# Kernel tuning notes

Measured on AMD Instinct MI355X. Metric: run time of the kernel, lower is better.

## Reference

```python
import jax, jax.numpy as jnp
import numpy as np

B, C, D, W, H = 8, 256, 24, 24, 24
COUT = 256
EMBED = 128
HEADS = 8
WORD = 64
POOL = 3  # forward hardcodes adaptive_avg_pool3d(x, 3)


def setup_inputs() -> dict:
    key = jax.random.key(0)
    ks = jax.random.split(key, 12)
    s = lambda n: 1.0 / np.sqrt(n)
    return {
        "x": jax.random.normal(ks[0], (B, C, D, W, H), dtype=jnp.float32),
        "qk_w": jax.random.normal(ks[1], (2 * EMBED, POOL ** 3), dtype=jnp.float32) * s(POOL ** 3),
        "qk_b": jax.random.normal(ks[2], (2 * EMBED,), dtype=jnp.float32) * 0.02,
        "wq_w": jax.random.normal(ks[3], (HEADS * WORD, EMBED), dtype=jnp.float32) * s(EMBED),
        "wq_b": jax.random.normal(ks[4], (HEADS * WORD,), dtype=jnp.float32) * 0.02,
        "wk_w": jax.random.normal(ks[5], (HEADS * WORD, EMBED), dtype=jnp.float32) * s(EMBED),
        "wk_b": jax.random.normal(ks[6], (HEADS * WORD,), dtype=jnp.float32) * 0.02,
        "fch_w": jax.random.normal(ks[7], (1, HEADS), dtype=jnp.float32) * s(HEADS),
        "fch_b": jax.random.normal(ks[8], (1,), dtype=jnp.float32) * 0.02,
        "conv_w": jax.random.normal(ks[9], (COUT, C), dtype=jnp.float32) * s(C),
        "conv_b": jax.random.normal(ks[10], (COUT,), dtype=jnp.float32) * 0.02,
    }


def reference(x, qk_w, qk_b, wq_w, wq_b, wk_w, wk_b, fch_w, fch_b, conv_w, conv_b):
    b, c, d, w, h = x.shape
    # adaptive_avg_pool3d to 3x3x3 (exact: dims divisible by 3) -> [b, c, 27]
    xmean = x.reshape(b, c, POOL, d // POOL, POOL, w // POOL, POOL, h // POOL)
    xmean = xmean.mean(axis=(3, 5, 7)).reshape(b, c, POOL ** 3)
    # qk projection -> split into q, k of [b, c, embed]
    qk = xmean @ qk_w.T + qk_b                      # [b, c, 2*embed]
    qk = qk.reshape(b, c, 2, EMBED)
    q, k = qk[:, :, 0], qk[:, :, 1]
    # head projections -> [b, heads, c, word]
    q = (q @ wq_w.T + wq_b).reshape(b, c, HEADS, WORD).transpose(0, 2, 1, 3)
    k = (k @ wk_w.T + wk_b).reshape(b, c, HEADS, WORD).transpose(0, 2, 1, 3)
    # channel attention: scores over channels [b, heads, c, c]
    scores = jnp.einsum("bhcw,bhkw->bhck", q / jnp.sqrt(jnp.float32(WORD)), k)
    attn = jax.nn.softmax(scores, axis=-1)          # dropout is identity in eval
    # v is the raw spatial map [b, c, d*w*h]; broadcast over heads
    v = x.reshape(b, c, d * w * h)
    y = jnp.einsum("bhck,bkn->bhcn", attn, v)       # [b, heads, c, dwh]
    # fch: Linear(heads, 1) combining heads
    y = jnp.einsum("bhcn,h->bcn", y, fch_w[0]) + fch_b[0]
    y = y.reshape(b, c, d, w, h)
    attn_out = jnp.einsum("bhck,h->bck", attn, fch_w[0]) + fch_b[0]  # [b, c, c]
    # 1x1x1 conv residual
    out = jnp.einsum("bcxyz,oc->boxyz", y + x, conv_w) + conv_b[None, :, None, None, None]
    return (out, attn_out)
```

## Files before the change

kernel.cpp:

```cpp
#include <hip/hip_runtime.h>
#include <cstdint>
#include <cstddef>

#define B_    8
#define C_    256
#define DWH   13824
#define P3    27
#define COUT_ 256

#define OFF_XMEAN 0
#define OFF_WQT   55296
#define OFF_WKT   69120
#define OFF_BQ    82944
#define OFF_BK    83456
#define OFF_BETA  83968
#define OFF_G     84224
#define OFF_U     90272
#define OFF_V     90488
#define OFF_D     90704
#define OFF_ZT    90712
#define OFF_A     549464
#define OFF_MPH   1073752
#define OFF_MPL   1335896

typedef __attribute__((ext_vector_type(8))) short bf16x8;
typedef __attribute__((ext_vector_type(4))) float f32x4;

__device__ __forceinline__ void split_bf16(float v, unsigned short& h, unsigned short& l) {
    unsigned u  = __float_as_uint(v);
    unsigned hu = u & 0xFFFF0000u;
    float r = v - __uint_as_float(hu);
    h = (unsigned short)(u >> 16);
    l = (unsigned short)(__float_as_uint(r) >> 16);
}

__device__ __forceinline__ unsigned rne2(float a, float b) {
    unsigned ua = __float_as_uint(a), ub = __float_as_uint(b);
    unsigned ra = (ua + 0x7FFFu + ((ua >> 16) & 1u)) >> 16;
    unsigned rb = (ub + 0x7FFFu + ((ub >> 16) & 1u)) >> 16;
    return ra | (rb << 16);
}

__global__ __launch_bounds__(256) void k_pool(const float* __restrict__ x,
                                              float* __restrict__ xmean) {
    int bc = blockIdx.x;
    __shared__ float p0[576], p1[576], p2[576];
    const float* xb = x + (size_t)bc * DWH;
    for (int t = threadIdx.x; t < 576; t += 256) {
        int g  = t >> 6;
        int s  = t & 63;
        int pd = g / 3, pw = g % 3;
        int d  = pd * 8 + (s >> 3);
        int w  = pw * 8 + (s & 7);
        const float4* r = (const float4*)(xb + ((size_t)d * 24 + w) * 24);
        float4 f0 = r[0], f1 = r[1], f2 = r[2], f3 = r[3], f4v = r[4], f5 = r[5];
        p0[t] = f0.x + f0.y + f0.z + f0.w + f1.x + f1.y + f1.z + f1.w;
        p1[t] = f2.x + f2.y + f2.z + f2.w + f3.x + f3.y + f3.z + f3.w;
        p2[t] = f4v.x + f4v.y + f4v.z + f4v.w + f5.x + f5.y + f5.z + f5.w;
    }
    __syncthreads();
    int tid = threadIdx.x;
    if (tid < 27) {
        int pd = tid / 9, pw = (tid / 3) % 3, ph = tid % 3;
        int g = pd * 3 + pw;
        const float* src = (ph == 0) ? p0 : (ph == 1 ? p1 : p2);
        float s = 0.f;
        #pragma unroll 8
        for (int i = 0; i < 64; ++i) s += src[g * 64 + i];
        xmean[(size_t)bc * P3 + tid] = s * (1.0f / 512.0f);
    }
}

__global__ __launch_bounds__(128) void k_combine(
    const float* __restrict__ qk_w, const float* __restrict__ qk_b,
    const float* __restrict__ wq_w, const float* __restrict__ wq_b,
    const float* __restrict__ wk_w, const float* __restrict__ wk_b,
    float* __restrict__ WqT, float* __restrict__ WkT,
    float* __restrict__ bq, float* __restrict__ bk) {
    int t = blockIdx.x * 128 + threadIdx.x;
    if (t < 13824) {
        int j = t / 27, p = t % 27;
        float s = 0.f;
        for (int e = 0; e < 128; ++e) s += wq_w[j * 128 + e] * qk_w[e * 27 + p];
        WqT[p * 512 + j] = s;
    } else if (t < 27648) {
        int u = t - 13824, j = u / 27, p = u % 27;
        float s = 0.f;
        for (int e = 0; e < 128; ++e) s += wk_w[j * 128 + e] * qk_w[(128 + e) * 27 + p];
        WkT[p * 512 + j] = s;
    } else if (t < 28160) {
        int j = t - 27648;
        float s = wq_b[j];
        for (int e = 0; e < 128; ++e) s += wq_w[j * 128 + e] * qk_b[e];
        bq[j] = s;
    } else if (t < 28672) {
        int j = t - 28160;
        float s = wk_b[j];
        for (int e = 0; e < 128; ++e) s += wk_w[j * 128 + e] * qk_b[128 + e];
        bk[j] = s;
    }
}

__global__ __launch_bounds__(256) void k_G(
    const float* __restrict__ WqT, const float* __restrict__ WkT,
    const float* __restrict__ bq, const float* __restrict__ bk,
    float* __restrict__ G, float* __restrict__ U,
    float* __restrict__ V, float* __restrict__ D) {
    int h = blockIdx.x;
    int base = h * 64;
    for (int idx = threadIdx.x; idx < 811; idx += 256) {
        if (idx < 756) {
            int p = idx / 28, r = idx % 28;
            float s = 0.f;
            if (r < 27)
                for (int w = 0; w < 64; ++w)
                    s += WqT[p * 512 + base + w] * WkT[r * 512 + base + w];
            G[(h * 27 + p) * 28 + r] = 0.125f * s;
        } else if (idx < 783) {
            int p = idx - 756;
            float s = 0.f;
            for (int w = 0; w < 64; ++w) s += WqT[p * 512 + base + w] * bk[base + w];
            V[h * 27 + p] = 0.125f * s;
        } else if (idx < 810) {
            int r = idx - 783;
            float s = 0.f;
            for (int w = 0; w < 64; ++w) s += WkT[r * 512 + base + w] * bq[base + w];
            U[h * 27 + r] = 0.125f * s;
        } else {
            float s = 0.f;
            for (int w = 0; w < 64; ++w) s += bq[base + w] * bk[base + w];
            D[h] = 0.125f * s;
        }
    }
}

__global__ __launch_bounds__(256) void k_z(
    const float* __restrict__ xmean, const float* __restrict__ G,
    const float* __restrict__ U, const float* __restrict__ V,
    const float* __restrict__ D, float* __restrict__ ZT) {
    int h = blockIdx.x, b = blockIdx.y;
    int k = threadIdx.x;
    __shared__ float Gs[756], Us[27], Vs[27], Ds;
    for (int idx = threadIdx.x; idx < 756; idx += 256) Gs[idx] = G[h * 756 + idx];
    if (threadIdx.x < 27) { Us[threadIdx.x] = U[h * 27 + threadIdx.x];
                            Vs[threadIdx.x] = V[h * 27 + threadIdx.x]; }
    if (threadIdx.x == 27) Ds = D[h];
    __syncthreads();
    float xm[28];
    const float* xp = xmean + ((size_t)(b * C_) + k) * P3;
    #pragma unroll
    for (int r = 0; r < 27; ++r) xm[r] = xp[r];
    xm[27] = 0.f;
    float z[28];
    #pragma unroll
    for (int p = 0; p < 27; ++p) {
        float acc = Vs[p];
        #pragma unroll
        for (int r4 = 0; r4 < 7; ++r4) {
            float4 g = *(const float4*)&Gs[p * 28 + r4 * 4];
            acc += g.x * xm[r4 * 4] + g.y * xm[r4 * 4 + 1]
                 + g.z * xm[r4 * 4 + 2] + g.w * xm[r4 * 4 + 3];
        }
        z[p] = acc;
    }
    {
        float e = Ds;
        #pragma unroll
        for (int r = 0; r < 27; ++r) e += Us[r] * xm[r];
        z[27] = e;
    }
    float4* zt = (float4*)ZT;
    int bh = b * 8 + h;
    #pragma unroll
    for (int p4 = 0; p4 < 7; ++p4) {
        float4 v = {z[p4 * 4], z[p4 * 4 + 1], z[p4 * 4 + 2], z[p4 * 4 + 3]};
        zt[((size_t)(bh * 7 + p4)) * 256 + k] = v;
    }
}

__global__ __launch_bounds__(256) void k_attn(
    const float* __restrict__ xmean, const float* __restrict__ ZT,
    const float* __restrict__ fch_w, const float* __restrict__ fch_b,
    float* __restrict__ A, float* __restrict__ attn_out) {
    int b = blockIdx.y;
    int c0 = blockIdx.x * 4;
    int t = threadIdx.x;
    int lane = t & 63, wv = t >> 6;
    __shared__ float xsh[4 * 28];
    __shared__ float ss[4][256];
    __shared__ float mx[4], den[4];
    if (t < 112) {
        int i = t / 28, p = t % 28;
        xsh[t] = (p < 27) ? xmean[((size_t)(b * C_) + c0 + i) * P3 + p] : 1.0f;
    }
    __syncthreads();
    float4 xr[4][7];
    #pragma unroll
    for (int cl = 0; cl < 4; ++cl)
        #pragma unroll
        for (int p4 = 0; p4 < 7; ++p4)
            xr[cl][p4] = *(const float4*)&xsh[cl * 28 + p4 * 4];
    float areg[4] = {0.f, 0.f, 0.f, 0.f};
    const float4* zt = (const float4*)ZT;
    for (int h = 0; h < 8; ++h) {
        int bh = b * 8 + h;
        float4 zk[7];
        #pragma unroll
        for (int p4 = 0; p4 < 7; ++p4)
            zk[p4] = zt[((size_t)(bh * 7 + p4)) * 256 + t];
        #pragma unroll
        for (int cl = 0; cl < 4; ++cl) {
            float dot = 0.f;
            #pragma unroll
            for (int p4 = 0; p4 < 7; ++p4) {
                float4 xv = xr[cl][p4];
                float4 zv = zk[p4];
                dot += xv.x * zv.x + xv.y * zv.y + xv.z * zv.z + xv.w * zv.w;
            }
            ss[cl][t] = dot;
        }
        __syncthreads();
        {
            int cl = wv;
            float4 v = *(const float4*)&ss[cl][lane * 4];
            float m = fmaxf(fmaxf(v.x, v.y), fmaxf(v.z, v.w));
            for (int off = 32; off; off >>= 1) m = fmaxf(m, __shfl_xor(m, off, 64));
            float s = expf(v.x - m) + expf(v.y - m) + expf(v.z - m) + expf(v.w - m);
            for (int off = 32; off; off >>= 1) s += __shfl_xor(s, off, 64);
            if (lane == 0) { mx[cl] = m; den[cl] = s; }
        }
        __syncthreads();
        float fw = fch_w[h];
        #pragma unroll
        for (int cl = 0; cl < 4; ++cl)
            areg[cl] += expf(ss[cl][t] - mx[cl]) * (fw / den[cl]);
        __syncthreads();
    }
    float fb = fch_b[0];
    #pragma unroll
    for (int cl = 0; cl < 4; ++cl) {
        size_t idx = ((size_t)(b * C_) + c0 + cl) * C_ + t;
        A[idx] = areg[cl];
        attn_out[idx] = areg[cl] + fb;
    }
}

__global__ __launch_bounds__(256) void k_M(
    const float* __restrict__ A, const float* __restrict__ conv_w,
    const float* __restrict__ fch_b, const float* __restrict__ conv_b,
    unsigned short* __restrict__ MpH, unsigned short* __restrict__ MpL,
    float* __restrict__ beta) {
    int b = blockIdx.y;
    int o0 = blockIdx.x * 8;
    int t = threadIdx.x;
    __shared__ float cw[8][256];
    #pragma unroll
    for (int r = 0; r < 8; ++r) cw[r][t] = conv_w[(o0 + r) * 256 + t];
    __syncthreads();
    float acc[8] = {0.f, 0.f, 0.f, 0.f, 0.f, 0.f, 0.f, 0.f};
    const float* Ab = A + (size_t)b * C_ * C_;
    for (int c = 0; c < 256; ++c) {
        float av = Ab[(size_t)c * 256 + t];
        #pragma unroll
        for (int r = 0; r < 8; ++r) acc[r] += cw[r][c] * av;
    }
    if (b == 0 && t < 8) {
        float s = 0.f;
        for (int c = 0; c < 256; ++c) s += cw[t][c];
        beta[o0 + t] = fch_b[0] * s + conv_b[o0 + t];
    }
    int ks = t >> 5, e = t & 7;
    int lanehi = ((t >> 3) & 3) << 4;
    size_t base = ((size_t)(b * 8 + ks) * 16 + (o0 >> 4)) * 64;
    int osub = (o0 & 8);
    #pragma unroll
    for (int r = 0; r < 8; ++r) {
        float mv = acc[r] + cw[r][t];
        unsigned short h, l;
        split_bf16(mv, h, l);
        size_t idx = (base + ((osub + r) | lanehi)) * 8 + e;
        MpH[idx] = h;
        MpL[idx] = l;
    }
}

__global__ __launch_bounds__(256, 3) void k_out_mfma(
    const bf16x8* __restrict__ MpH, const bf16x8* __restrict__ MpL,
    const float* __restrict__ x, const float* __restrict__ beta,
    float* __restrict__ out) {
    int b  = blockIdx.y;
    int n0 = blockIdx.x * 64;
    int t  = threadIdx.x;
    int lane = t & 63, wv = t >> 6;
    int l15  = lane & 15;
    int kseg = lane >> 4;

    __shared__ __align__(16) unsigned short Xs[2][64 * 32];

    f32x4 acc[4][4];
    #pragma unroll
    for (int m = 0; m < 4; ++m)
        #pragma unroll
        for (int nf = 0; nf < 4; ++nf) acc[m][nf] = (f32x4){0.f, 0.f, 0.f, 0.f};

    const float* xb = x + (size_t)b * 256 * DWH;
    const bf16x8* mh = MpH + (size_t)b * 8192;
    const bf16x8* ml = MpL + (size_t)b * 8192;

    int sn = t & 63;
    int sk = t >> 6;
    const float* xcol0 = xb + (size_t)(sk * 8) * DWH + n0 + sn;
    int soff = sn * 64 + ((sk * 16) ^ (((sn >> 1) & 3) << 4));

    {
        float xr[8];
        #pragma unroll
        for (int j = 0; j < 8; ++j) xr[j] = xcol0[(size_t)j * DWH];
        uint4 v;
        v.x = rne2(xr[0], xr[1]); v.y = rne2(xr[2], xr[3]);
        v.z = rne2(xr[4], xr[5]); v.w = rne2(xr[6], xr[7]);
        *(uint4*)((char*)Xs[0] + soff) = v;
    }
    __syncthreads();

    for (int s = 0; s < 8; ++s) {
        int cur = s & 1;
        float xn[8];
        if (s < 7) {
            const float* xc = xcol0 + (size_t)((s + 1) * 32) * DWH;
            #pragma unroll
            for (int j = 0; j < 8; ++j) xn[j] = xc[(size_t)j * DWH];
        }
        bf16x8 Ah[4], Al[4];
        #pragma unroll
        for (int m = 0; m < 4; ++m) {
            int idx = (s * 16 + wv * 4 + m) * 64 + lane;
            Ah[m] = mh[idx];
            Al[m] = ml[idx];
        }
        bf16x8 Bf[4];
        #pragma unroll
        for (int nf = 0; nf < 4; ++nf) {
            int n = nf * 16 + l15;
            int off = n * 64 + ((kseg * 16) ^ (((n >> 1) & 3) << 4));
            Bf[nf] = *(const bf16x8*)((const char*)Xs[cur] + off);
        }
        #pragma unroll
        for (int m = 0; m < 4; ++m)
            #pragma unroll
            for (int nf = 0; nf < 4; ++nf) {
                f32x4 c = acc[m][nf];
                c = __builtin_amdgcn_mfma_f32_16x16x32_bf16(Al[m], Bf[nf], c, 0, 0, 0);
                c = __builtin_amdgcn_mfma_f32_16x16x32_bf16(Ah[m], Bf[nf], c, 0, 0, 0);
                acc[m][nf] = c;
            }
        if (s < 7) {
            uint4 v;
            v.x = rne2(xn[0], xn[1]); v.y = rne2(xn[2], xn[3]);
            v.z = rne2(xn[4], xn[5]); v.w = rne2(xn[6], xn[7]);
            *(uint4*)((char*)Xs[cur ^ 1] + soff) = v;
        }
        __syncthreads();
    }

    int r4 = (lane >> 4) * 4;
    int wo = wv * 64;
    #pragma unroll
    for (int m = 0; m < 4; ++m) {
        int obase = wo + m * 16 + r4;
        float bet[4];
        #pragma unroll
        for (int r = 0; r < 4; ++r) bet[r] = beta[obase + r];
        #pragma unroll
        for (int nf = 0; nf < 4; ++nf) {
            int n = n0 + nf * 16 + l15;
            #pragma unroll
            for (int r = 0; r < 4; ++r)
                out[((size_t)(b * 256 + obase + r)) * DWH + n] = acc[m][nf][r] + bet[r];
        }
    }
}

extern "C" void kernel_launch(void* const* d_in, const int* in_sizes, int n_in,
                              void* d_out, int out_size, void* d_ws, size_t ws_size,
                              hipStream_t stream) {
    const float* x      = (const float*)d_in[0];
    const float* qk_w   = (const float*)d_in[1];
    const float* qk_b   = (const float*)d_in[2];
    const float* wq_w   = (const float*)d_in[3];
    const float* wq_b   = (const float*)d_in[4];
    const float* wk_w   = (const float*)d_in[5];
    const float* wk_b   = (const float*)d_in[6];
    const float* fch_w  = (const float*)d_in[7];
    const float* fch_b  = (const float*)d_in[8];
    const float* conv_w = (const float*)d_in[9];
    const float* conv_b = (const float*)d_in[10];
    float* out = (float*)d_out;
    float* attn_out = out + (size_t)B_ * COUT_ * DWH;
    float* ws = (float*)d_ws;
    unsigned short* MpH = (unsigned short*)(ws + OFF_MPH);
    unsigned short* MpL = (unsigned short*)(ws + OFF_MPL);

    k_pool<<<B_ * C_, 256, 0, stream>>>(x, ws + OFF_XMEAN);
    k_combine<<<224, 128, 0, stream>>>(qk_w, qk_b, wq_w, wq_b, wk_w, wk_b,
                                       ws + OFF_WQT, ws + OFF_WKT,
                                       ws + OFF_BQ, ws + OFF_BK);
    k_G<<<8, 256, 0, stream>>>(ws + OFF_WQT, ws + OFF_WKT, ws + OFF_BQ, ws + OFF_BK,
                               ws + OFF_G, ws + OFF_U, ws + OFF_V, ws + OFF_D);
    k_z<<<dim3(8, B_), 256, 0, stream>>>(ws + OFF_XMEAN, ws + OFF_G, ws + OFF_U,
                                         ws + OFF_V, ws + OFF_D, ws + OFF_ZT);
    k_attn<<<dim3(64, B_), 256, 0, stream>>>(ws + OFF_XMEAN, ws + OFF_ZT, fch_w, fch_b,
                                             ws + OFF_A, attn_out);
    k_M<<<dim3(32, B_), 256, 0, stream>>>(ws + OFF_A, conv_w, fch_b, conv_b,
                                          MpH, MpL, ws + OFF_BETA);
    k_out_mfma<<<dim3(216, B_), 256, 0, stream>>>((const bf16x8*)MpH, (const bf16x8*)MpL,
                                                  x, ws + OFF_BETA, out);
}
```

Baseline: 132.0 us.

## Fuse G and z kernels, parallelize pool reduction, batch softmax across heads

Merges k_G into k_z so each (head, batch) block recomputes the head's G/U/V/D terms from shared-memory copies of the combined weights, removing one launch and the global round trip for G. The pool kernel's final 27-cell reduction is split across 216 threads with a second shared-memory stage instead of 27 serial threads. The attention kernel stores scores for all 8 heads in shared memory and does the softmax reductions in one pass, cutting the per-head barriers. The cost is redundant G computation across the 8 batch blocks and more shared memory in k_attn.

```diff
diff --git a/kernel.cpp b/kernel.cpp
--- a/kernel.cpp
+++ b/kernel.cpp
@@ -14,10 +14,6 @@
 #define OFF_BQ    82944
 #define OFF_BK    83456
 #define OFF_BETA  83968
-#define OFF_G     84224
-#define OFF_U     90272
-#define OFF_V     90488
-#define OFF_D     90704
 #define OFF_ZT    90712
 #define OFF_A     549464
 #define OFF_MPH   1073752
@@ -45,6 +41,7 @@
                                               float* __restrict__ xmean) {
     int bc = blockIdx.x;
     __shared__ float p0[576], p1[576], p2[576];
+    __shared__ float part[216];
     const float* xb = x + (size_t)bc * DWH;
     for (int t = threadIdx.x; t < 576; t += 256) {
         int g  = t >> 6;
@@ -60,13 +57,21 @@
     }
     __syncthreads();
     int tid = threadIdx.x;
-    if (tid < 27) {
-        int pd = tid / 9, pw = (tid / 3) % 3, ph = tid % 3;
+    if (tid < 216) {
+        int cell = tid >> 3, seg = tid & 7;
+        int pd = cell / 9, pw = (cell / 3) % 3, ph = cell % 3;
         int g = pd * 3 + pw;
         const float* src = (ph == 0) ? p0 : (ph == 1 ? p1 : p2);
         float s = 0.f;
-        #pragma unroll 8
-        for (int i = 0; i < 64; ++i) s += src[g * 64 + i];
+        #pragma unroll
+        for (int i = 0; i < 8; ++i) s += src[g * 64 + seg * 8 + i];
+        part[tid] = s;
+    }
+    __syncthreads();
+    if (tid < 27) {
+        float s = 0.f;
+        #pragma unroll
+        for (int i = 0; i < 8; ++i) s += part[tid * 8 + i];
         xmean[(size_t)bc * P3 + tid] = s * (1.0f / 512.0f);
     }
 }
@@ -101,51 +106,47 @@
     }
 }
 
-__global__ __launch_bounds__(256) void k_G(
+__global__ __launch_bounds__(256) void k_zG(
     const float* __restrict__ WqT, const float* __restrict__ WkT,
     const float* __restrict__ bq, const float* __restrict__ bk,
-    float* __restrict__ G, float* __restrict__ U,
-    float* __restrict__ V, float* __restrict__ D) {
-    int h = blockIdx.x;
-    int base = h * 64;
-    for (int idx = threadIdx.x; idx < 811; idx += 256) {
+    const float* __restrict__ xmean, float* __restrict__ ZT) {
+    int h = blockIdx.x, b = blockIdx.y;
+    int t = threadIdx.x;
+    __shared__ float Wq[P3][65], Wk[P3][65];
+    __shared__ float bqs[64], bks[64];
+    __shared__ float Gs[756], Us[P3], Vs[P3], Ds;
+    for (int idx = t; idx < 1728; idx += 256) {
+        int p = idx >> 6, w = idx & 63;
+        Wq[p][w] = WqT[p * 512 + h * 64 + w];
+        Wk[p][w] = WkT[p * 512 + h * 64 + w];
+    }
+    if (t < 64) { bqs[t] = bq[h * 64 + t]; bks[t] = bk[h * 64 + t]; }
+    __syncthreads();
+    for (int idx = t; idx < 811; idx += 256) {
         if (idx < 756) {
             int p = idx / 28, r = idx % 28;
             float s = 0.f;
             if (r < 27)
-                for (int w = 0; w < 64; ++w)
-                    s += WqT[p * 512 + base + w] * WkT[r * 512 + base + w];
-            G[(h * 27 + p) * 28 + r] = 0.125f * s;
+                for (int w = 0; w < 64; ++w) s += Wq[p][w] * Wk[r][w];
+            Gs[p * 28 + r] = 0.125f * s;
         } else if (idx < 783) {
             int p = idx - 756;
             float s = 0.f;
-            for (int w = 0; w < 64; ++w) s += WqT[p * 512 + base + w] * bk[base + w];
-            V[h * 27 + p] = 0.125f * s;
+            for (int w = 0; w < 64; ++w) s += Wq[p][w] * bks[w];
+            Vs[p] = 0.125f * s;
         } else if (idx < 810) {
             int r = idx - 783;
             float s = 0.f;
-            for (int w = 0; w < 64; ++w) s += WkT[r * 512 + base + w] * bq[base + w];
-            U[h * 27 + r] = 0.125f * s;
+            for (int w = 0; w < 64; ++w) s += Wk[r][w] * bqs[w];
+            Us[r] = 0.125f * s;
         } else {
             float s = 0.f;
-            for (int w = 0; w < 64; ++w) s += bq[base + w] * bk[base + w];
-            D[h] = 0.125f * s;
-        }
-    }
-}
-
-__global__ __launch_bounds__(256) void k_z(
-    const float* __restrict__ xmean, const float* __restrict__ G,
-    const float* __restrict__ U, const float* __restrict__ V,
-    const float* __restrict__ D, float* __restrict__ ZT) {
-    int h = blockIdx.x, b = blockIdx.y;
-    int k = threadIdx.x;
-    __shared__ float Gs[756], Us[27], Vs[27], Ds;
-    for (int idx = threadIdx.x; idx < 756; idx += 256) Gs[idx] = G[h * 756 + idx];
-    if (threadIdx.x < 27) { Us[threadIdx.x] = U[h * 27 + threadIdx.x];
-                            Vs[threadIdx.x] = V[h * 27 + threadIdx.x]; }
-    if (threadIdx.x == 27) Ds = D[h];
-    __syncthreads();
+            for (int w = 0; w < 64; ++w) s += bqs[w] * bks[w];
+            Ds = 0.125f * s;
+        }
+    }
+    __syncthreads();
+    int k = t;
     float xm[28];
     const float* xp = xmean + ((size_t)(b * C_) + k) * P3;
     #pragma unroll
@@ -187,20 +188,13 @@
     int t = threadIdx.x;
     int lane = t & 63, wv = t >> 6;
     __shared__ float xsh[4 * 28];
-    __shared__ float ss[4][256];
-    __shared__ float mx[4], den[4];
+    __shared__ float ss[8][4][256];
+    __shared__ float mx[8][4], scl[8][4];
     if (t < 112) {
         int i = t / 28, p = t % 28;
         xsh[t] = (p < 27) ? xmean[((size_t)(b * C_) + c0 + i) * P3 + p] : 1.0f;
     }
     __syncthreads();
-    float4 xr[4][7];
-    #pragma unroll
-    for (int cl = 0; cl < 4; ++cl)
-        #pragma unroll
-        for (int p4 = 0; p4 < 7; ++p4)
-            xr[cl][p4] = *(const float4*)&xsh[cl * 28 + p4 * 4];
-    float areg[4] = {0.f, 0.f, 0.f, 0.f};
     const float4* zt = (const float4*)ZT;
     for (int h = 0; h < 8; ++h) {
         int bh = b * 8 + h;
@@ -213,29 +207,32 @@
             float dot = 0.f;
             #pragma unroll
             for (int p4 = 0; p4 < 7; ++p4) {
-                float4 xv = xr[cl][p4];
+                float4 xv = *(const float4*)&xsh[cl * 28 + p4 * 4];
                 float4 zv = zk[p4];
                 dot += xv.x * zv.x + xv.y * zv.y + xv.z * zv.z + xv.w * zv.w;
             }
-            ss[cl][t] = dot;
-        }
-        __syncthreads();
-        {
-            int cl = wv;
-            float4 v = *(const float4*)&ss[cl][lane * 4];
-            float m = fmaxf(fmaxf(v.x, v.y), fmaxf(v.z, v.w));
-            for (int off = 32; off; off >>= 1) m = fmaxf(m, __shfl_xor(m, off, 64));
-            float s = expf(v.x - m) + expf(v.y - m) + expf(v.z - m) + expf(v.w - m);
-            for (int off = 32; off; off >>= 1) s += __shfl_xor(s, off, 64);
-            if (lane == 0) { mx[cl] = m; den[cl] = s; }
-        }
-        __syncthreads();
-        float fw = fch_w[h];
+            ss[h][cl][t] = dot;
+        }
+    }
+    __syncthreads();
+    #pragma unroll
+    for (int j = 0; j < 8; ++j) {
+        int pr = wv * 8 + j;
+        int h = pr >> 2, cl = pr & 3;
+        float4 v = *(const float4*)&ss[h][cl][lane * 4];
+        float m = fmaxf(fmaxf(v.x, v.y), fmaxf(v.z, v.w));
+        for (int off = 32; off; off >>= 1) m = fmaxf(m, __shfl_xor(m, off, 64));
+        float s = expf(v.x - m) + expf(v.y - m) + expf(v.z - m) + expf(v.w - m);
+        for (int off = 32; off; off >>= 1) s += __shfl_xor(s, off, 64);
+        if (lane == 0) { mx[h][cl] = m; scl[h][cl] = fch_w[h] / s; }
+    }
+    __syncthreads();
+    float areg[4] = {0.f, 0.f, 0.f, 0.f};
+    #pragma unroll
+    for (int h = 0; h < 8; ++h)
         #pragma unroll
         for (int cl = 0; cl < 4; ++cl)
-            areg[cl] += expf(ss[cl][t] - mx[cl]) * (fw / den[cl]);
-        __syncthreads();
-    }
+            areg[cl] += expf(ss[h][cl][t] - mx[h][cl]) * scl[h][cl];
     float fb = fch_b[0];
     #pragma unroll
     for (int cl = 0; cl < 4; ++cl) {
@@ -405,10 +402,9 @@
     k_combine<<<224, 128, 0, stream>>>(qk_w, qk_b, wq_w, wq_b, wk_w, wk_b,
                                        ws + OFF_WQT, ws + OFF_WKT,
                                        ws + OFF_BQ, ws + OFF_BK);
-    k_G<<<8, 256, 0, stream>>>(ws + OFF_WQT, ws + OFF_WKT, ws + OFF_BQ, ws + OFF_BK,
-                               ws + OFF_G, ws + OFF_U, ws + OFF_V, ws + OFF_D);
-    k_z<<<dim3(8, B_), 256, 0, stream>>>(ws + OFF_XMEAN, ws + OFF_G, ws + OFF_U,
-                                         ws + OFF_V, ws + OFF_D, ws + OFF_ZT);
+    k_zG<<<dim3(8, B_), 256, 0, stream>>>(ws + OFF_WQT, ws + OFF_WKT,
+                                          ws + OFF_BQ, ws + OFF_BK,
+                                          ws + OFF_XMEAN, ws + OFF_ZT);
     k_attn<<<dim3(64, B_), 256, 0, stream>>>(ws + OFF_XMEAN, ws + OFF_ZT, fch_w, fch_b,
                                              ws + OFF_A, attn_out);
     k_M<<<dim3(32, B_), 256, 0, stream>>>(ws + OFF_A, conv_w, fch_b, conv_b,
```

Measured after the change: 143.2 us. +8.5%, slower.
